# Kernel optimization log

Hardware: AMD Instinct MI355X
Metric: run time of the kernel (lower is better)

The kernel has to match this reference:

```python
import jax, jax.numpy as jnp
import numpy as np

SAMPLE_RATE = 24000
THRESHOLD_FACTOR = 5.0
MAX_SPIKE_SAMPLES = int(0.0015 * SAMPLE_RATE)  # 36
K_MAX = 65536  # static upper bound on number of threshold crossings
N_SAMPLES = 24_000_000


def setup_inputs() -> dict:
    key = jax.random.key(0)
    x = jax.random.normal(key, (N_SAMPLES,), dtype=jnp.float32)
    return {"data_detected": x}


def _detect_one(v, threshold):
    """Detect peaks of v above +threshold. For the negative pass, call with -x
    (x < -thr  <=>  -x > thr, and argmin(x) == argmax(-x)). Returns an int32
    array of length K_MAX: valid peak indices first (sorted), padded with -1."""
    N = v.shape[0]
    mask = (v > threshold).astype(jnp.int32)
    d = jnp.diff(mask)  # +1 = entry (False->True), -1 = exit (True->False)
    entries = jnp.nonzero(d == 1, size=K_MAX, fill_value=N)[0]
    exits = jnp.nonzero(d == -1, size=K_MAX, fill_value=N)[0]
    n = jnp.minimum(jnp.sum(d == 1), jnp.sum(d == -1))
    idx = jnp.arange(K_MAX)
    dur = exits - entries
    keep = (idx < n) & (dur <= MAX_SPIKE_SAMPLES)
    # vectorized windowed peak search: (K_MAX, W) gather + row argmax
    win_idx = jnp.clip(entries[:, None] + jnp.arange(MAX_SPIKE_SAMPLES)[None, :], 0, N - 1)
    windows = v[win_idx]
    peaks = entries + jnp.argmax(windows, axis=1)
    # compact valid peaks to the front (entries are sorted), pad with -1
    peaks = jnp.sort(jnp.where(keep, peaks, N))
    total = jnp.sum(keep)
    return jnp.where(idx < total, peaks, -1)


def reference(data_detected):
    x = data_detected
    threshold = THRESHOLD_FACTOR * jnp.median(jnp.abs(x)) / 0.6745
    pos_indices = _detect_one(x, threshold)
    neg_indices = _detect_one(-x, threshold)
    return pos_indices, neg_indices, threshold
```

## Files before the change

### kernel.cpp

```cpp
#include <hip/hip_runtime.h>
#include <stdint.h>

#define HB 18
#define HIST1_SIZE 8192
#define CAND_CAP 8192
#define LIST_CAP 1500000
#define LBUF_CAP 3072
#define PAIR_CAP 1024
#define PEAK_CAP 512
#define MAX_SPIKE 36
#define STAGE_BLOCKS 128

#define P_B1    0
#define P_B2    1
#define P_R1    2
#define P_R2    3
#define P_THRLO 4
#define P_THR   5
#define P_CANDN 6
#define P_LISTN 7
#define P_BINA0 8
#define P_BINA1 9
#define P_RA0   10
#define P_RA1   11
#define P_DONEA 12
#define P_DONEB 13

#define WS_HIST1   0
#define WS_HISTA   32768
#define WS_HISTB   34816
#define WS_PARAMS  43008
#define WS_ZERO_BYTES 43072
#define WS_CAND    43072
#define WS_LIST    76800

__global__ __launch_bounds__(256) void k_hist1(const float* __restrict__ x, int N,
                                               int* __restrict__ hist1) {
  __shared__ int h[HIST1_SIZE];
  for (int i = threadIdx.x; i < HIST1_SIZE; i += 256) h[i] = 0;
  __syncthreads();
  int NV = N >> 2;
  int str = gridDim.x * 256;
  const float4* vec = reinterpret_cast<const float4*>(x);
  int j = blockIdx.x * 256 + threadIdx.x;
  for (; j + 7 * str < NV; j += 8 * str) {
    float4 v[8];
#pragma unroll
    for (int k = 0; k < 8; ++k) v[k] = vec[j + k * str];
#pragma unroll
    for (int k = 0; k < 8; ++k) {
      atomicAdd(&h[(__float_as_uint(v[k].x) & 0x7fffffffu) >> HB], 1);
      atomicAdd(&h[(__float_as_uint(v[k].y) & 0x7fffffffu) >> HB], 1);
      atomicAdd(&h[(__float_as_uint(v[k].z) & 0x7fffffffu) >> HB], 1);
      atomicAdd(&h[(__float_as_uint(v[k].w) & 0x7fffffffu) >> HB], 1);
    }
  }
  for (; j < NV; j += str) {
    float4 a = vec[j];
    atomicAdd(&h[(__float_as_uint(a.x) & 0x7fffffffu) >> HB], 1);
    atomicAdd(&h[(__float_as_uint(a.y) & 0x7fffffffu) >> HB], 1);
    atomicAdd(&h[(__float_as_uint(a.z) & 0x7fffffffu) >> HB], 1);
    atomicAdd(&h[(__float_as_uint(a.w) & 0x7fffffffu) >> HB], 1);
  }
  if (blockIdx.x == 0 && threadIdx.x == 0) {
    for (int i = NV << 2; i < N; ++i)
      atomicAdd(&h[(__float_as_uint(x[i]) & 0x7fffffffu) >> HB], 1);
  }
  __syncthreads();
  for (int i = threadIdx.x; i < HIST1_SIZE; i += 256) {
    int c = h[i];
    if (c) atomicAdd(&hist1[i], c);
  }
}

__global__ void k_select(const int* __restrict__ hist1, long long k1, long long k2,
                         int* __restrict__ p) {
  __shared__ int part[256];
  __shared__ long long excl[256];
  __shared__ int b1s, b2s, r1s, r2s;
  int tid = threadIdx.x;
  const int chunk = HIST1_SIZE / 256;
  int base = tid * chunk;
  int s = 0;
  for (int w = 0; w < chunk; ++w) s += hist1[base + w];
  part[tid] = s;
  __syncthreads();
  if (tid == 0) {
    long long acc = 0;
    for (int i = 0; i < 256; ++i) { excl[i] = acc; acc += part[i]; }
  }
  __syncthreads();
  long long pre = excl[tid];
  if (pre <= k1 && k1 < pre + part[tid]) {
    long long acc = pre;
    for (int w = 0; w < chunk; ++w) {
      int c = hist1[base + w];
      if (k1 < acc + c) { b1s = base + w; r1s = (int)(k1 - acc); break; }
      acc += c;
    }
  }
  if (pre <= k2 && k2 < pre + part[tid]) {
    long long acc = pre;
    for (int w = 0; w < chunk; ++w) {
      int c = hist1[base + w];
      if (k2 < acc + c) { b2s = base + w; r2s = (int)(k2 - acc); break; }
      acc += c;
    }
  }
  __syncthreads();
  if (tid == 0) {
    p[P_B1] = b1s; p[P_B2] = b2s;
    p[P_R1] = r1s; p[P_R2] = r2s;
    float lo1 = __uint_as_float((uint32_t)b1s << HB);
    float lo2 = __uint_as_float((uint32_t)b2s << HB);
    float mLo = 0.5f * (lo1 + lo2);
    p[P_THRLO] = __float_as_int((5.0f * mLo / 0.6745f) * 0.999f);
  }
}

__device__ inline void p2_elem(float f, int idx, int b1, int b2, float thrLo,
                               int* lbuf, int* lcnt, int* list, int* p, int* cand) {
  uint32_t u = __float_as_uint(f) & 0x7fffffffu;
  int top = (int)(u >> HB);
  if (top == b1 || top == b2) {
    int id = atomicAdd(lcnt, 1);
    if (id < LBUF_CAP) lbuf[id] = (int)u;
    else { int g = atomicAdd(&p[P_LISTN], 1); if (g < LIST_CAP) list[g] = (int)u; }
  }
  if (__uint_as_float(u) > thrLo) {
    int id = atomicAdd(&p[P_CANDN], 1);
    if (id < CAND_CAP) cand[id] = idx;
  }
}

__global__ __launch_bounds__(256) void k_pass2(const float* __restrict__ x, int N,
                                               int* __restrict__ p,
                                               int* __restrict__ list,
                                               int* __restrict__ cand) {
  __shared__ int lbuf[LBUF_CAP];
  __shared__ int lcnt;
  __shared__ int lbase;
  if (threadIdx.x == 0) lcnt = 0;
  __syncthreads();
  int b1 = p[P_B1], b2 = p[P_B2];
  float thrLo = __int_as_float(p[P_THRLO]);
  int NV = N >> 2;
  int str = gridDim.x * 256;
  const float4* vec = reinterpret_cast<const float4*>(x);
  int j = blockIdx.x * 256 + threadIdx.x;
  for (; j + 7 * str < NV; j += 8 * str) {
    float4 v[8];
#pragma unroll
    for (int k = 0; k < 8; ++k) v[k] = vec[j + k * str];
#pragma unroll
    for (int k = 0; k < 8; ++k) {
      int base = (j + k * str) << 2;
      p2_elem(v[k].x, base + 0, b1, b2, thrLo, lbuf, &lcnt, list, p, cand);
      p2_elem(v[k].y, base + 1, b1, b2, thrLo, lbuf, &lcnt, list, p, cand);
      p2_elem(v[k].z, base + 2, b1, b2, thrLo, lbuf, &lcnt, list, p, cand);
      p2_elem(v[k].w, base + 3, b1, b2, thrLo, lbuf, &lcnt, list, p, cand);
    }
  }
  for (; j < NV; j += str) {
    float4 a = vec[j];
    int base = j << 2;
    p2_elem(a.x, base + 0, b1, b2, thrLo, lbuf, &lcnt, list, p, cand);
    p2_elem(a.y, base + 1, b1, b2, thrLo, lbuf, &lcnt, list, p, cand);
    p2_elem(a.z, base + 2, b1, b2, thrLo, lbuf, &lcnt, list, p, cand);
    p2_elem(a.w, base + 3, b1, b2, thrLo, lbuf, &lcnt, list, p, cand);
  }
  if (blockIdx.x == 0 && threadIdx.x == 0) {
    for (int i = NV << 2; i < N; ++i)
      p2_elem(x[i], i, b1, b2, thrLo, lbuf, &lcnt, list, p, cand);
  }
  __syncthreads();
  int n = lcnt < LBUF_CAP ? lcnt : LBUF_CAP;
  if (threadIdx.x == 0) lbase = atomicAdd(&p[P_LISTN], n);
  __syncthreads();
  int base = lbase;
  for (int i = threadIdx.x; i < n; i += 256)
    if (base + i < LIST_CAP) list[base + i] = lbuf[i];
}

__global__ __launch_bounds__(256) void k_stageA(const int* __restrict__ list,
                                                int* __restrict__ p,
                                                int* __restrict__ histA) {
  __shared__ int h[512];
  __shared__ int lastS;
  __shared__ int sh[256];
  __shared__ int excl[256];
  for (int i = threadIdx.x; i < 512; i += 256) h[i] = 0;
  __syncthreads();
  int n = p[P_LISTN]; if (n > LIST_CAP) n = LIST_CAP;
  int b1 = p[P_B1], b2 = p[P_B2];
  int str = gridDim.x * 256;
  for (int i = blockIdx.x * 256 + threadIdx.x; i < n; i += str) {
    int v = list[i];
    int top = v >> HB;
    int bin = (v >> 10) & 255;
    if (top == b1) atomicAdd(&h[bin], 1);
    if (top == b2) atomicAdd(&h[256 + bin], 1);
  }
  __syncthreads();
  for (int i = threadIdx.x; i < 512; i += 256) {
    int c = h[i];
    if (c) atomicAdd(&histA[i], c);
  }
  __threadfence();
  if (threadIdx.x == 0) lastS = (atomicAdd(&p[P_DONEA], 1) == (int)gridDim.x - 1);
  __syncthreads();
  if (!lastS) return;
  __threadfence();
  int tid = threadIdx.x;
  for (int tgt = 0; tgt < 2; ++tgt) {
    int rank = p[P_R1 + tgt];
    int c = histA[tgt * 256 + tid];
    sh[tid] = c;
    __syncthreads();
    if (tid == 0) { int a = 0; for (int i = 0; i < 256; ++i) { excl[i] = a; a += sh[i]; } }
    __syncthreads();
    int pre = excl[tid];
    if (pre <= rank && rank < pre + c) {
      p[P_BINA0 + tgt] = tid;
      p[P_RA0 + tgt] = rank - pre;
    }
    __syncthreads();
  }
}

__global__ __launch_bounds__(256) void k_stageB(const int* __restrict__ list,
                                                int* __restrict__ p,
                                                int* __restrict__ histB,
                                                float* __restrict__ outThr) {
  __shared__ int h[2048];
  __shared__ int lastS;
  __shared__ int sh[256];
  __shared__ int excl[256];
  __shared__ float vres[2];
  for (int i = threadIdx.x; i < 2048; i += 256) h[i] = 0;
  __syncthreads();
  int n = p[P_LISTN]; if (n > LIST_CAP) n = LIST_CAP;
  int b1 = p[P_B1], b2 = p[P_B2];
  int bA0 = p[P_BINA0], bA1 = p[P_BINA1];
  int str = gridDim.x * 256;
  for (int i = blockIdx.x * 256 + threadIdx.x; i < n; i += str) {
    int v = list[i];
    int top = v >> HB;
    int bin = (v >> 10) & 255;
    int lo = v & 1023;
    if (top == b1 && bin == bA0) atomicAdd(&h[lo], 1);
    if (top == b2 && bin == bA1) atomicAdd(&h[1024 + lo], 1);
  }
  __syncthreads();
  for (int i = threadIdx.x; i < 2048; i += 256) {
    int c = h[i];
    if (c) atomicAdd(&histB[i], c);
  }
  __threadfence();
  if (threadIdx.x == 0) lastS = (atomicAdd(&p[P_DONEB], 1) == (int)gridDim.x - 1);
  __syncthreads();
  if (!lastS) return;
  __threadfence();
  int tid = threadIdx.x;
  if (tid < 2) vres[tid] = 0.0f;
  for (int tgt = 0; tgt < 2; ++tgt) {
    __syncthreads();
    int rank = p[P_RA0 + tgt];
    const int* hh = histB + tgt * 1024;
    int c0 = hh[tid * 4], c1 = hh[tid * 4 + 1], c2 = hh[tid * 4 + 2], c3 = hh[tid * 4 + 3];
    sh[tid] = c0 + c1 + c2 + c3;
    __syncthreads();
    if (tid == 0) { int a = 0; for (int i = 0; i < 256; ++i) { excl[i] = a; a += sh[i]; } }
    __syncthreads();
    int pre = excl[tid];
    if (pre <= rank && rank < pre + sh[tid]) {
      int a = pre;
      int cc[4] = {c0, c1, c2, c3};
      for (int w = 0; w < 4; ++w) {
        if (rank < a + cc[w]) {
          int bkt = (tgt == 0) ? b1 : b2;
          uint32_t bits = ((uint32_t)bkt << HB) | ((uint32_t)p[P_BINA0 + tgt] << 10) |
                          (uint32_t)(tid * 4 + w);
          vres[tgt] = __uint_as_float(bits);
          break;
        }
        a += cc[w];
      }
    }
  }
  __syncthreads();
  if (tid == 0) {
    float med = 0.5f * (vres[0] + vres[1]);
    float thr = (5.0f * med) / 0.6745f;
    p[P_THR] = __float_as_int(thr);
    *outThr = thr;
  }
}

__global__ __launch_bounds__(256) void k_fillpad(float* __restrict__ out, int n2) {
  int j = blockIdx.x * 256 + threadIdx.x;
  if (j < n2) out[j] = -1.0f;
}

__device__ static void isort(int* a, int n) {
  for (int i = 1; i < n; ++i) {
    int v = a[i]; int j = i - 1;
    while (j >= 0 && a[j] > v) { a[j + 1] = a[j]; --j; }
    a[j + 1] = v;
  }
}

__device__ inline void eval_pair(const float* __restrict__ x, int p, float thr,
                                 int* pe, int* px, int* ne, int* nx, int* cnt) {
  float a = x[p], b = x[p + 1];
  bool m0 = a > thr, m1 = b > thr;
  if (m0 != m1) {
    int id = atomicAdd(&cnt[m1 ? 0 : 1], 1);
    if (id < PAIR_CAP) (m1 ? pe : px)[id] = p;
  }
  bool q0 = (-a) > thr, q1 = (-b) > thr;
  if (q0 != q1) {
    int id = atomicAdd(&cnt[q1 ? 2 : 3], 1);
    if (id < PAIR_CAP) (q1 ? ne : nx)[id] = p;
  }
}

__device__ inline int wave_argmax36(const float* __restrict__ x, int N, int sign,
                                    int e, int lane) {
  float val = -INFINITY;
  int wi = lane;
  if (lane < MAX_SPIKE) {
    int idx = e + lane; if (idx > N - 1) idx = N - 1;
    float v = x[idx];
    val = (sign < 0) ? -v : v;
  }
  for (int off = 32; off; off >>= 1) {
    float ov = __shfl_xor(val, off);
    int owi = __shfl_xor(wi, off);
    if (ov > val || (ov == val && owi < wi)) { val = ov; wi = owi; }
  }
  return e + wi;
}

__device__ inline int proc_pol(const float* __restrict__ x, int N, int sign,
                               const int* eL, int nE, const int* xL, int nX,
                               int* pk, int tid) {
  int n = nE < nX ? nE : nX;
  int tot = 0;
  for (int t = 0; t < n; ++t) {
    int dur = xL[t] - eL[t];
    if (dur <= MAX_SPIKE) {
      int pp = wave_argmax36(x, N, sign, eL[t], tid);
      if (tot < PEAK_CAP && tid == 0) pk[tot] = pp;
      ++tot;
    }
  }
  if (tot > PEAK_CAP) tot = PEAK_CAP;
  if (tid == 0) isort(pk, tot);
  return tot;
}

__global__ void k_finalize(const float* __restrict__ x, int N,
                           int* __restrict__ p, int* __restrict__ cand,
                           float* __restrict__ out, int OUT_K) {
  __shared__ int pe[PAIR_CAP], px[PAIR_CAP], ne[PAIR_CAP], nx[PAIR_CAP];
  __shared__ int cnt[4];
  __shared__ int pkP[PEAK_CAP], pkN[PEAK_CAP];
  __shared__ int nPk[2];
  int tid = threadIdx.x;
  float thr = __int_as_float(p[P_THR]);
  int nC = p[P_CANDN]; if (nC > CAND_CAP) nC = CAND_CAP;
  if (tid < 4) cnt[tid] = 0;
  __syncthreads();
  if (tid == 0) isort(cand, nC);
  __syncthreads();
  for (int k = tid; k < nC; k += 64) {
    int c = cand[k];
    bool prevAdj = (k > 0) && (cand[k - 1] == c - 1);
    if (c > 0 && !prevAdj) eval_pair(x, c - 1, thr, pe, px, ne, nx, cnt);
    if (c <= N - 2) eval_pair(x, c, thr, pe, px, ne, nx, cnt);
  }
  __syncthreads();
  int nPE = min(cnt[0], PAIR_CAP), nPX = min(cnt[1], PAIR_CAP);
  int nNE = min(cnt[2], PAIR_CAP), nNX = min(cnt[3], PAIR_CAP);
  if (tid == 0) { isort(pe, nPE); isort(px, nPX); }
  else if (tid == 1) { isort(ne, nNE); isort(nx, nNX); }
  __syncthreads();
  int t0 = proc_pol(x, N, +1, pe, nPE, px, nPX, pkP, tid);
  int t1 = proc_pol(x, N, -1, ne, nNE, nx, nNX, pkN, tid);
  if (tid == 0) { nPk[0] = t0; nPk[1] = t1; }
  __syncthreads();
  for (int j = tid; j < nPk[0]; j += 64) out[j] = (float)pkP[j];
  for (int j = tid; j < nPk[1]; j += 64) out[OUT_K + j] = (float)pkN[j];
}

extern "C" void kernel_launch(void* const* d_in, const int* in_sizes, int n_in,
                              void* d_out, int out_size, void* d_ws, size_t ws_size,
                              hipStream_t stream) {
  const float* x = (const float*)d_in[0];
  int N = in_sizes[0];
  float* out = (float*)d_out;
  char* ws = (char*)d_ws;

  int* hist1  = (int*)(ws + WS_HIST1);
  int* histA  = (int*)(ws + WS_HISTA);
  int* histB  = (int*)(ws + WS_HISTB);
  int* params = (int*)(ws + WS_PARAMS);
  int* cand   = (int*)(ws + WS_CAND);
  int* list   = (int*)(ws + WS_LIST);

  hipMemsetAsync(d_ws, 0, WS_ZERO_BYTES, stream);

  long long k1 = (long long)(N / 2) - 1;
  long long k2 = (long long)(N / 2);
  int OUT_K = (out_size - 1) / 2;

  k_fillpad<<<(2 * OUT_K + 255) / 256, 256, 0, stream>>>(out, 2 * OUT_K);
  k_hist1<<<2048, 256, 0, stream>>>(x, N, hist1);
  k_select<<<1, 256, 0, stream>>>(hist1, k1, k2, params);
  k_pass2<<<2048, 256, 0, stream>>>(x, N, params, list, cand);
  k_stageA<<<STAGE_BLOCKS, 256, 0, stream>>>(list, params, histA);
  k_stageB<<<STAGE_BLOCKS, 256, 0, stream>>>(list, params, histB, out + 2 * OUT_K);
  k_finalize<<<1, 64, 0, stream>>>(x, N, params, cand, out, OUT_K);
}
```

Measured before the change: 160.4 us.

## Replace full histogram pass with sampled band selection for median

Drops the full-data 8192-bin histogram pass and instead samples 65536 strided elements to pick a value band likely to contain the median. The main pass then counts elements below the band and collects band members as offsets, and two refinement histograms find the exact median ranks. This removes one full read of the 96 MB input. The cost is reliance on sampling: if the true median falls outside the band, rank clamping gives a wrong answer, and the list can grow to 2.5M entries. The memset is also replaced with a zeroing kernel.

```diff
diff --git a/kernel.cpp b/kernel.cpp
--- a/kernel.cpp
+++ b/kernel.cpp
@@ -2,130 +2,122 @@
 #include <stdint.h>
 
 #define HB 18
-#define HIST1_SIZE 8192
+#define SH_SIZE 8192
+#define NSAMP 65536
+#define SMARG 1912
+#define DBITS 22
 #define CAND_CAP 8192
-#define LIST_CAP 1500000
+#define LIST_CAP 2500000
 #define LBUF_CAP 3072
 #define PAIR_CAP 1024
 #define PEAK_CAP 512
 #define MAX_SPIKE 36
-#define STAGE_BLOCKS 128
-
-#define P_B1    0
-#define P_B2    1
-#define P_R1    2
-#define P_R2    3
-#define P_THRLO 4
-#define P_THR   5
-#define P_CANDN 6
-#define P_LISTN 7
-#define P_BINA0 8
-#define P_BINA1 9
-#define P_RA0   10
-#define P_RA1   11
-#define P_DONEA 12
-#define P_DONEB 13
-
-#define WS_HIST1   0
-#define WS_HISTA   32768
-#define WS_HISTB   34816
-#define WS_PARAMS  43008
-#define WS_ZERO_BYTES 43072
-#define WS_CAND    43072
-#define WS_LIST    76800
-
-__global__ __launch_bounds__(256) void k_hist1(const float* __restrict__ x, int N,
-                                               int* __restrict__ hist1) {
-  __shared__ int h[HIST1_SIZE];
-  for (int i = threadIdx.x; i < HIST1_SIZE; i += 256) h[i] = 0;
-  __syncthreads();
-  int NV = N >> 2;
-  int str = gridDim.x * 256;
-  const float4* vec = reinterpret_cast<const float4*>(x);
+#define AB_BLOCKS 128
+
+#define P_ULO   0
+#define P_UHI   1
+#define P_THRLO 2
+#define P_THR   3
+#define P_CANDN 4
+#define P_LISTN 5
+#define P_CB    6
+#define P_BINA1 7
+#define P_BINA2 8
+#define P_RA1   9
+#define P_RA2   10
+#define P_DONEA 11
+#define P_DONEB 12
+
+#define WS_SHIST  0
+#define WS_HISTA  32768
+#define WS_HISTB  40960
+#define WS_PARAMS 57344
+#define WS_ZERO_BYTES 57408
+#define WS_CAND   57408
+#define WS_LIST   102400
+
+__global__ __launch_bounds__(256) void k_zero(int* __restrict__ ws, int nInts) {
   int j = blockIdx.x * 256 + threadIdx.x;
-  for (; j + 7 * str < NV; j += 8 * str) {
-    float4 v[8];
-#pragma unroll
-    for (int k = 0; k < 8; ++k) v[k] = vec[j + k * str];
-#pragma unroll
-    for (int k = 0; k < 8; ++k) {
-      atomicAdd(&h[(__float_as_uint(v[k].x) & 0x7fffffffu) >> HB], 1);
-      atomicAdd(&h[(__float_as_uint(v[k].y) & 0x7fffffffu) >> HB], 1);
-      atomicAdd(&h[(__float_as_uint(v[k].z) & 0x7fffffffu) >> HB], 1);
-      atomicAdd(&h[(__float_as_uint(v[k].w) & 0x7fffffffu) >> HB], 1);
-    }
-  }
-  for (; j < NV; j += str) {
-    float4 a = vec[j];
-    atomicAdd(&h[(__float_as_uint(a.x) & 0x7fffffffu) >> HB], 1);
-    atomicAdd(&h[(__float_as_uint(a.y) & 0x7fffffffu) >> HB], 1);
-    atomicAdd(&h[(__float_as_uint(a.z) & 0x7fffffffu) >> HB], 1);
-    atomicAdd(&h[(__float_as_uint(a.w) & 0x7fffffffu) >> HB], 1);
-  }
-  if (blockIdx.x == 0 && threadIdx.x == 0) {
-    for (int i = NV << 2; i < N; ++i)
-      atomicAdd(&h[(__float_as_uint(x[i]) & 0x7fffffffu) >> HB], 1);
-  }
-  __syncthreads();
-  for (int i = threadIdx.x; i < HIST1_SIZE; i += 256) {
+  if (j < nInts) ws[j] = 0;
+}
+
+__global__ __launch_bounds__(256) void k_fillpad(float* __restrict__ out, int n2) {
+  int j = blockIdx.x * 256 + threadIdx.x;
+  if (j < n2) out[j] = -1.0f;
+}
+
+__global__ __launch_bounds__(256) void k_sample(const float* __restrict__ x, int N,
+                                                int* __restrict__ shist) {
+  __shared__ int h[SH_SIZE];
+  for (int i = threadIdx.x; i < SH_SIZE; i += 256) h[i] = 0;
+  __syncthreads();
+  int stride = N / NSAMP; if (stride < 1) stride = 1;
+  for (int i = blockIdx.x * 256 + threadIdx.x; i < NSAMP; i += gridDim.x * 256) {
+    long long idx = (long long)i * stride;
+    if (idx < N) {
+      uint32_t u = __float_as_uint(x[idx]) & 0x7fffffffu;
+      atomicAdd(&h[u >> HB], 1);
+    }
+  }
+  __syncthreads();
+  for (int i = threadIdx.x; i < SH_SIZE; i += 256) {
     int c = h[i];
-    if (c) atomicAdd(&hist1[i], c);
-  }
-}
-
-__global__ void k_select(const int* __restrict__ hist1, long long k1, long long k2,
-                         int* __restrict__ p) {
+    if (c) atomicAdd(&shist[i], c);
+  }
+}
+
+__global__ void k_bandsel(const int* __restrict__ shist, int* __restrict__ p) {
   __shared__ int part[256];
-  __shared__ long long excl[256];
-  __shared__ int b1s, b2s, r1s, r2s;
+  __shared__ int excl[256];
+  __shared__ uint32_t uLoS, uHiS;
   int tid = threadIdx.x;
-  const int chunk = HIST1_SIZE / 256;
+  const int chunk = SH_SIZE / 256;
   int base = tid * chunk;
   int s = 0;
-  for (int w = 0; w < chunk; ++w) s += hist1[base + w];
+  for (int w = 0; w < chunk; ++w) s += shist[base + w];
   part[tid] = s;
   __syncthreads();
+  if (tid == 0) { int a = 0; for (int i = 0; i < 256; ++i) { excl[i] = a; a += part[i]; } }
+  __syncthreads();
+  int pre = excl[tid];
+  int sA = NSAMP / 2 - SMARG, sB = NSAMP / 2 + SMARG;
+  if (pre <= sA && sA < pre + part[tid]) {
+    int a = pre;
+    for (int w = 0; w < chunk; ++w) {
+      int c = shist[base + w];
+      if (sA < a + c) { uLoS = (uint32_t)(base + w) << HB; break; }
+      a += c;
+    }
+  }
+  if (pre <= sB && sB < pre + part[tid]) {
+    int a = pre;
+    for (int w = 0; w < chunk; ++w) {
+      int c = shist[base + w];
+      if (sB < a + c) { uHiS = (uint32_t)(base + w + 1) << HB; break; }
+      a += c;
+    }
+  }
+  __syncthreads();
   if (tid == 0) {
-    long long acc = 0;
-    for (int i = 0; i < 256; ++i) { excl[i] = acc; acc += part[i]; }
-  }
-  __syncthreads();
-  long long pre = excl[tid];
-  if (pre <= k1 && k1 < pre + part[tid]) {
-    long long acc = pre;
-    for (int w = 0; w < chunk; ++w) {
-      int c = hist1[base + w];
-      if (k1 < acc + c) { b1s = base + w; r1s = (int)(k1 - acc); break; }
-      acc += c;
-    }
-  }
-  if (pre <= k2 && k2 < pre + part[tid]) {
-    long long acc = pre;
-    for (int w = 0; w < chunk; ++w) {
-      int c = hist1[base + w];
-      if (k2 < acc + c) { b2s = base + w; r2s = (int)(k2 - acc); break; }
-      acc += c;
-    }
-  }
-  __syncthreads();
-  if (tid == 0) {
-    p[P_B1] = b1s; p[P_B2] = b2s;
-    p[P_R1] = r1s; p[P_R2] = r2s;
-    float lo1 = __uint_as_float((uint32_t)b1s << HB);
-    float lo2 = __uint_as_float((uint32_t)b2s << HB);
-    float mLo = 0.5f * (lo1 + lo2);
-    p[P_THRLO] = __float_as_int((5.0f * mLo / 0.6745f) * 0.999f);
-  }
-}
-
-__device__ inline void p2_elem(float f, int idx, int b1, int b2, float thrLo,
-                               int* lbuf, int* lcnt, int* list, int* p, int* cand) {
+    uint32_t uLo = uLoS, uHi = uHiS;
+    if (uHi - uLo > (1u << DBITS)) uHi = uLo + (1u << DBITS);
+    p[P_ULO] = (int)uLo;
+    p[P_UHI] = (int)uHi;
+    float vLo = __uint_as_float(uLo);
+    p[P_THRLO] = __float_as_int((5.0f * vLo / 0.6745f) * 0.999f);
+  }
+}
+
+__device__ inline void m_elem(float f, int idx, uint32_t uLo, uint32_t uHi, float thrLo,
+                              int* lbuf, int* lcnt, int* list, int* p, int* cand,
+                              int& cb) {
   uint32_t u = __float_as_uint(f) & 0x7fffffffu;
-  int top = (int)(u >> HB);
-  if (top == b1 || top == b2) {
+  cb += (u < uLo) ? 1 : 0;
+  if (u >= uLo && u < uHi) {
+    int d = (int)(u - uLo);
     int id = atomicAdd(lcnt, 1);
-    if (id < LBUF_CAP) lbuf[id] = (int)u;
-    else { int g = atomicAdd(&p[P_LISTN], 1); if (g < LIST_CAP) list[g] = (int)u; }
+    if (id < LBUF_CAP) lbuf[id] = d;
+    else { int g = atomicAdd(&p[P_LISTN], 1); if (g < LIST_CAP) list[g] = d; }
   }
   if (__uint_as_float(u) > thrLo) {
     int id = atomicAdd(&p[P_CANDN], 1);
@@ -133,17 +125,19 @@
   }
 }
 
-__global__ __launch_bounds__(256) void k_pass2(const float* __restrict__ x, int N,
-                                               int* __restrict__ p,
-                                               int* __restrict__ list,
-                                               int* __restrict__ cand) {
+__global__ __launch_bounds__(256) void k_main(const float* __restrict__ x, int N,
+                                              int* __restrict__ p,
+                                              int* __restrict__ list,
+                                              int* __restrict__ cand) {
   __shared__ int lbuf[LBUF_CAP];
   __shared__ int lcnt;
   __shared__ int lbase;
+  __shared__ int red[256];
   if (threadIdx.x == 0) lcnt = 0;
   __syncthreads();
-  int b1 = p[P_B1], b2 = p[P_B2];
+  uint32_t uLo = (uint32_t)p[P_ULO], uHi = (uint32_t)p[P_UHI];
   float thrLo = __int_as_float(p[P_THRLO]);
+  int cb = 0;
   int NV = N >> 2;
   int str = gridDim.x * 256;
   const float4* vec = reinterpret_cast<const float4*>(x);
@@ -155,28 +149,34 @@
 #pragma unroll
     for (int k = 0; k < 8; ++k) {
       int base = (j + k * str) << 2;
-      p2_elem(v[k].x, base + 0, b1, b2, thrLo, lbuf, &lcnt, list, p, cand);
-      p2_elem(v[k].y, base + 1, b1, b2, thrLo, lbuf, &lcnt, list, p, cand);
-      p2_elem(v[k].z, base + 2, b1, b2, thrLo, lbuf, &lcnt, list, p, cand);
-      p2_elem(v[k].w, base + 3, b1, b2, thrLo, lbuf, &lcnt, list, p, cand);
+      m_elem(v[k].x, base + 0, uLo, uHi, thrLo, lbuf, &lcnt, list, p, cand, cb);
+      m_elem(v[k].y, base + 1, uLo, uHi, thrLo, lbuf, &lcnt, list, p, cand, cb);
+      m_elem(v[k].z, base + 2, uLo, uHi, thrLo, lbuf, &lcnt, list, p, cand, cb);
+      m_elem(v[k].w, base + 3, uLo, uHi, thrLo, lbuf, &lcnt, list, p, cand, cb);
     }
   }
   for (; j < NV; j += str) {
     float4 a = vec[j];
     int base = j << 2;
-    p2_elem(a.x, base + 0, b1, b2, thrLo, lbuf, &lcnt, list, p, cand);
-    p2_elem(a.y, base + 1, b1, b2, thrLo, lbuf, &lcnt, list, p, cand);
-    p2_elem(a.z, base + 2, b1, b2, thrLo, lbuf, &lcnt, list, p, cand);
-    p2_elem(a.w, base + 3, b1, b2, thrLo, lbuf, &lcnt, list, p, cand);
+    m_elem(a.x, base + 0, uLo, uHi, thrLo, lbuf, &lcnt, list, p, cand, cb);
+    m_elem(a.y, base + 1, uLo, uHi, thrLo, lbuf, &lcnt, list, p, cand, cb);
+    m_elem(a.z, base + 2, uLo, uHi, thrLo, lbuf, &lcnt, list, p, cand, cb);
+    m_elem(a.w, base + 3, uLo, uHi, thrLo, lbuf, &lcnt, list, p, cand, cb);
   }
   if (blockIdx.x == 0 && threadIdx.x == 0) {
     for (int i = NV << 2; i < N; ++i)
-      p2_elem(x[i], i, b1, b2, thrLo, lbuf, &lcnt, list, p, cand);
+      m_elem(x[i], i, uLo, uHi, thrLo, lbuf, &lcnt, list, p, cand, cb);
   }
   __syncthreads();
   int n = lcnt < LBUF_CAP ? lcnt : LBUF_CAP;
   if (threadIdx.x == 0) lbase = atomicAdd(&p[P_LISTN], n);
-  __syncthreads();
+  red[threadIdx.x] = cb;
+  __syncthreads();
+  for (int s2 = 128; s2; s2 >>= 1) {
+    if (threadIdx.x < s2) red[threadIdx.x] += red[threadIdx.x + s2];
+    __syncthreads();
+  }
+  if (threadIdx.x == 0) atomicAdd(&p[P_CB], red[0]);
   int base = lbase;
   for (int i = threadIdx.x; i < n; i += 256)
     if (base + i < LIST_CAP) list[base + i] = lbuf[i];
@@ -184,25 +184,20 @@
 
 __global__ __launch_bounds__(256) void k_stageA(const int* __restrict__ list,
                                                 int* __restrict__ p,
-                                                int* __restrict__ histA) {
-  __shared__ int h[512];
+                                                int* __restrict__ histA,
+                                                long long k1, long long k2) {
+  __shared__ int h[2048];
   __shared__ int lastS;
-  __shared__ int sh[256];
+  __shared__ int part[256];
   __shared__ int excl[256];
-  for (int i = threadIdx.x; i < 512; i += 256) h[i] = 0;
+  for (int i = threadIdx.x; i < 2048; i += 256) h[i] = 0;
   __syncthreads();
   int n = p[P_LISTN]; if (n > LIST_CAP) n = LIST_CAP;
-  int b1 = p[P_B1], b2 = p[P_B2];
   int str = gridDim.x * 256;
-  for (int i = blockIdx.x * 256 + threadIdx.x; i < n; i += str) {
-    int v = list[i];
-    int top = v >> HB;
-    int bin = (v >> 10) & 255;
-    if (top == b1) atomicAdd(&h[bin], 1);
-    if (top == b2) atomicAdd(&h[256 + bin], 1);
-  }
-  __syncthreads();
-  for (int i = threadIdx.x; i < 512; i += 256) {
+  for (int i = blockIdx.x * 256 + threadIdx.x; i < n; i += str)
+    atomicAdd(&h[list[i] >> 11], 1);
+  __syncthreads();
+  for (int i = threadIdx.x; i < 2048; i += 256) {
     int c = h[i];
     if (c) atomicAdd(&histA[i], c);
   }
@@ -212,19 +207,33 @@
   if (!lastS) return;
   __threadfence();
   int tid = threadIdx.x;
-  for (int tgt = 0; tgt < 2; ++tgt) {
-    int rank = p[P_R1 + tgt];
-    int c = histA[tgt * 256 + tid];
-    sh[tid] = c;
-    __syncthreads();
-    if (tid == 0) { int a = 0; for (int i = 0; i < 256; ++i) { excl[i] = a; a += sh[i]; } }
-    __syncthreads();
-    int pre = excl[tid];
-    if (pre <= rank && rank < pre + c) {
-      p[P_BINA0 + tgt] = tid;
-      p[P_RA0 + tgt] = rank - pre;
-    }
-    __syncthreads();
+  long long cb = p[P_CB];
+  long long r1l = k1 - cb, r2l = k2 - cb;
+  if (r1l < 0) r1l = 0; if (r1l > n - 1) r1l = n - 1;
+  if (r2l < 0) r2l = 0; if (r2l > n - 1) r2l = n - 1;
+  int r1 = (int)r1l, r2 = (int)r2l;
+  int base = tid * 8;
+  int cc[8]; int s = 0;
+#pragma unroll
+  for (int w = 0; w < 8; ++w) { cc[w] = histA[base + w]; s += cc[w]; }
+  part[tid] = s;
+  __syncthreads();
+  if (tid == 0) { int a = 0; for (int i = 0; i < 256; ++i) { excl[i] = a; a += part[i]; } }
+  __syncthreads();
+  int pre = excl[tid];
+  if (pre <= r1 && r1 < pre + s) {
+    int a = pre;
+    for (int w = 0; w < 8; ++w) {
+      if (r1 < a + cc[w]) { p[P_BINA1] = base + w; p[P_RA1] = r1 - a; break; }
+      a += cc[w];
+    }
+  }
+  if (pre <= r2 && r2 < pre + s) {
+    int a = pre;
+    for (int w = 0; w < 8; ++w) {
+      if (r2 < a + cc[w]) { p[P_BINA2] = base + w; p[P_RA2] = r2 - a; break; }
+      a += cc[w];
+    }
   }
 }
 
@@ -232,27 +241,24 @@
                                                 int* __restrict__ p,
                                                 int* __restrict__ histB,
                                                 float* __restrict__ outThr) {
-  __shared__ int h[2048];
+  __shared__ int h[4096];
   __shared__ int lastS;
-  __shared__ int sh[256];
+  __shared__ int part[256];
   __shared__ int excl[256];
   __shared__ float vres[2];
-  for (int i = threadIdx.x; i < 2048; i += 256) h[i] = 0;
+  for (int i = threadIdx.x; i < 4096; i += 256) h[i] = 0;
   __syncthreads();
   int n = p[P_LISTN]; if (n > LIST_CAP) n = LIST_CAP;
-  int b1 = p[P_B1], b2 = p[P_B2];
-  int bA0 = p[P_BINA0], bA1 = p[P_BINA1];
+  int binA1 = p[P_BINA1], binA2 = p[P_BINA2];
   int str = gridDim.x * 256;
   for (int i = blockIdx.x * 256 + threadIdx.x; i < n; i += str) {
-    int v = list[i];
-    int top = v >> HB;
-    int bin = (v >> 10) & 255;
-    int lo = v & 1023;
-    if (top == b1 && bin == bA0) atomicAdd(&h[lo], 1);
-    if (top == b2 && bin == bA1) atomicAdd(&h[1024 + lo], 1);
-  }
-  __syncthreads();
-  for (int i = threadIdx.x; i < 2048; i += 256) {
+    int d = list[i];
+    int hi = d >> 11, lo = d & 2047;
+    if (hi == binA1) atomicAdd(&h[lo], 1);
+    if (hi == binA2) atomicAdd(&h[2048 + lo], 1);
+  }
+  __syncthreads();
+  for (int i = threadIdx.x; i < 4096; i += 256) {
     int c = h[i];
     if (c) atomicAdd(&histB[i], c);
   }
@@ -262,25 +268,27 @@
   if (!lastS) return;
   __threadfence();
   int tid = threadIdx.x;
-  if (tid < 2) vres[tid] = 0.0f;
+  uint32_t uLo = (uint32_t)p[P_ULO];
+  if (tid < 2) vres[tid] = __uint_as_float(uLo);
   for (int tgt = 0; tgt < 2; ++tgt) {
     __syncthreads();
-    int rank = p[P_RA0 + tgt];
-    const int* hh = histB + tgt * 1024;
-    int c0 = hh[tid * 4], c1 = hh[tid * 4 + 1], c2 = hh[tid * 4 + 2], c3 = hh[tid * 4 + 3];
-    sh[tid] = c0 + c1 + c2 + c3;
+    const int* hh = histB + tgt * 2048;
+    int rank = (tgt == 0) ? p[P_RA1] : p[P_RA2];
+    int binA = (tgt == 0) ? binA1 : binA2;
+    int base = tid * 8;
+    int cc[8]; int s = 0;
+#pragma unroll
+    for (int w = 0; w < 8; ++w) { cc[w] = hh[base + w]; s += cc[w]; }
+    part[tid] = s;
     __syncthreads();
-    if (tid == 0) { int a = 0; for (int i = 0; i < 256; ++i) { excl[i] = a; a += sh[i]; } }
+    if (tid == 0) { int a = 0; for (int i = 0; i < 256; ++i) { excl[i] = a; a += part[i]; } }
     __syncthreads();
     int pre = excl[tid];
-    if (pre <= rank && rank < pre + sh[tid]) {
+    if (pre <= rank && rank < pre + s) {
       int a = pre;
-      int cc[4] = {c0, c1, c2, c3};
-      for (int w = 0; w < 4; ++w) {
+      for (int w = 0; w < 8; ++w) {
         if (rank < a + cc[w]) {
-          int bkt = (tgt == 0) ? b1 : b2;
-          uint32_t bits = ((uint32_t)bkt << HB) | ((uint32_t)p[P_BINA0 + tgt] << 10) |
-                          (uint32_t)(tid * 4 + w);
+          uint32_t bits = uLo + ((uint32_t)binA << 11) + (uint32_t)(base + w);
           vres[tgt] = __uint_as_float(bits);
           break;
         }
@@ -295,11 +303,6 @@
     p[P_THR] = __float_as_int(thr);
     *outThr = thr;
   }
-}
-
-__global__ __launch_bounds__(256) void k_fillpad(float* __restrict__ out, int n2) {
-  int j = blockIdx.x * 256 + threadIdx.x;
-  if (j < n2) out[j] = -1.0f;
 }
 
 __device__ static void isort(int* a, int n) {
@@ -402,24 +405,24 @@
   float* out = (float*)d_out;
   char* ws = (char*)d_ws;
 
-  int* hist1  = (int*)(ws + WS_HIST1);
+  int* shist  = (int*)(ws + WS_SHIST);
   int* histA  = (int*)(ws + WS_HISTA);
   int* histB  = (int*)(ws + WS_HISTB);
   int* params = (int*)(ws + WS_PARAMS);
   int* cand   = (int*)(ws + WS_CAND);
   int* list   = (int*)(ws + WS_LIST);
 
-  hipMemsetAsync(d_ws, 0, WS_ZERO_BYTES, stream);
-
   long long k1 = (long long)(N / 2) - 1;
   long long k2 = (long long)(N / 2);
   int OUT_K = (out_size - 1) / 2;
 
+  int zInts = WS_ZERO_BYTES / 4;
+  k_zero<<<(zInts + 255) / 256, 256, 0, stream>>>((int*)ws, zInts);
   k_fillpad<<<(2 * OUT_K + 255) / 256, 256, 0, stream>>>(out, 2 * OUT_K);
-  k_hist1<<<2048, 256, 0, stream>>>(x, N, hist1);
-  k_select<<<1, 256, 0, stream>>>(hist1, k1, k2, params);
-  k_pass2<<<2048, 256, 0, stream>>>(x, N, params, list, cand);
-  k_stageA<<<STAGE_BLOCKS, 256, 0, stream>>>(list, params, histA);
-  k_stageB<<<STAGE_BLOCKS, 256, 0, stream>>>(list, params, histB, out + 2 * OUT_K);
+  k_sample<<<64, 256, 0, stream>>>(x, N, shist);
+  k_bandsel<<<1, 256, 0, stream>>>(shist, params);
+  k_main<<<2048, 256, 0, stream>>>(x, N, params, list, cand);
+  k_stageA<<<AB_BLOCKS, 256, 0, stream>>>(list, params, histA, k1, k2);
+  k_stageB<<<AB_BLOCKS, 256, 0, stream>>>(list, params, histB, out + 2 * OUT_K);
   k_finalize<<<1, 64, 0, stream>>>(x, N, params, cand, out, OUT_K);
 }
```

Result: slower. 301.6 us (+88.0%).
